# Kernel optimization log

Measured on AMD Instinct MI355X. Metric: run time of the kernel, lower is better.

The kernel has to match this reference:

```python
import jax, jax.numpy as jnp
import numpy as np

OUT_F = 4096
IN_F = 4096
NUM_BITS = 4
BLOCK = 64
R = 16
LORA_SCALE = 32.0 / R  # lora_alpha / r


def setup_inputs() -> dict:
    key = jax.random.key(0)
    k1, k2, k3, k4, k5, k6 = jax.random.split(key, 6)
    n_packed = OUT_F * IN_F * NUM_BITS // 8  # bytes; 2 nibbles per byte
    n_blocks = OUT_F * IN_F // BLOCK
    return {
        "x": jax.random.normal(k1, (2, 1024, IN_F), dtype=jnp.float32),
        "qweight": jax.random.randint(k2, (n_packed,), 0, 256, dtype=jnp.int32),
        "scales": jax.random.uniform(k3, (n_blocks,), dtype=jnp.float32),
        "bias": jax.random.normal(k4, (OUT_F,), dtype=jnp.float32),
        "lora_A": jax.random.normal(k5, (R, IN_F), dtype=jnp.float32) * 0.02,
        "lora_B": jax.random.normal(k6, (OUT_F, R), dtype=jnp.float32) * 0.02,
    }


def _dequantize(qweight, scales):
    # uniform 4-bit lookup table: linspace(-1, 1, 16)
    table = jnp.linspace(-1.0, 1.0, 2 ** NUM_BITS).astype(scales.dtype)
    mask = (1 << NUM_BITS) - 1
    # unpack: index i stored at bits [i*NUM_BITS, (i+1)*NUM_BITS) of each byte
    lo = qweight & mask
    hi = (qweight >> NUM_BITS) & mask
    idx = jnp.stack([lo, hi], axis=-1).reshape(-1)  # [OUT_F*IN_F]
    vals = table[idx]                                # gather from lookup table
    # per-block rescale, then reshape to [OUT_F, IN_F]
    w = vals.reshape(-1, BLOCK) * scales[:, None]
    return w.reshape(OUT_F, IN_F)


def reference(x, qweight, scales, bias, lora_A, lora_B):
    W = _dequantize(qweight, scales)                      # [out, in]
    base = jnp.einsum('bsi,oi->bso', x, W) + bias          # F.linear
    lora = jnp.einsum('bsr,or->bso', jnp.einsum('bsi,ri->bsr', x, lora_A), lora_B)
    return base + LORA_SCALE * lora
```

## Files before the change

kernel.cpp:

```cpp
#include <hip/hip_runtime.h>
#include <hip/hip_bf16.h>
#include <stdint.h>

#define IN_F   4096
#define OUT_F  4096
#define M_ROWS 2048
#define LORA_SCALE 2.0f

typedef __bf16 bf16x8 __attribute__((ext_vector_type(8)));
typedef float  f32x4  __attribute__((ext_vector_type(4)));

typedef const __attribute__((address_space(1))) void gvoid_t;
typedef __attribute__((address_space(3))) void lvoid_t;

__global__ void prep_kernel(const int* __restrict__ qw,
                            const float* __restrict__ scales,
                            __hip_bfloat16* __restrict__ W,
                            const float* __restrict__ x,
                            __hip_bfloat16* __restrict__ xb,
                            const float* __restrict__ A,
                            float* __restrict__ tout) {
    int b = blockIdx.x;
    if (b < 8192) {
        int t = b * 256 + threadIdx.x;
        int4 q = ((const int4*)qw)[t];
        float scale = scales[t >> 3];
        float step = scale * (2.0f / 15.0f);
        int bb[4] = {q.x, q.y, q.z, q.w};
        union { __hip_bfloat16 h[8]; uint4 v; } o;
        #pragma unroll
        for (int j = 0; j < 4; ++j) {
            float lo = (float)(bb[j] & 15)        * step - scale;
            float hi = (float)((bb[j] >> 4) & 15) * step - scale;
            o.h[2*j]   = __float2bfloat16(lo);
            o.h[2*j+1] = __float2bfloat16(hi);
        }
        ((uint4*)W)[t] = o.v;
    } else if (b < 12288) {
        int t = (b - 8192) * 256 + threadIdx.x;
        float4 a = ((const float4*)x)[2*t];
        float4 c = ((const float4*)x)[2*t + 1];
        union { __hip_bfloat16 h[8]; uint4 v; } o;
        o.h[0] = __float2bfloat16(a.x); o.h[1] = __float2bfloat16(a.y);
        o.h[2] = __float2bfloat16(a.z); o.h[3] = __float2bfloat16(a.w);
        o.h[4] = __float2bfloat16(c.x); o.h[5] = __float2bfloat16(c.y);
        o.h[6] = __float2bfloat16(c.z); o.h[7] = __float2bfloat16(c.w);
        ((uint4*)xb)[t] = o.v;
    } else {
        __shared__ float red[16 * 4 * 16];
        int m0 = (b - 12288) * 4;
        int r = threadIdx.x & 15;
        int g = threadIdx.x >> 4;
        float acc[4] = {0.f, 0.f, 0.f, 0.f};
        for (int kb = 0; kb < 64; ++kb) {
            int k = kb * 64 + g * 4;
            float4 av = *(const float4*)(A + (size_t)r * IN_F + k);
            #pragma unroll
            for (int row = 0; row < 4; ++row) {
                float4 xv = *(const float4*)(x + (size_t)(m0 + row) * IN_F + k);
                acc[row] += xv.x*av.x + xv.y*av.y + xv.z*av.z + xv.w*av.w;
            }
        }
        #pragma unroll
        for (int row = 0; row < 4; ++row) red[g*64 + row*16 + r] = acc[row];
        __syncthreads();
        if (threadIdx.x < 64) {
            int row = threadIdx.x >> 4, rr = threadIdx.x & 15;
            float s = 0.f;
            #pragma unroll
            for (int gg = 0; gg < 16; ++gg) s += red[gg*64 + row*16 + rr];
            tout[(size_t)(m0 + row) * 16 + rr] = s;
        }
    }
}

__global__ __launch_bounds__(256) void gemm_kernel(
        const __hip_bfloat16* __restrict__ A,
        const __hip_bfloat16* __restrict__ B,
        const float* __restrict__ bias,
        const float* __restrict__ loraB,
        const float* __restrict__ tmat,
        float* __restrict__ out) {
    const int K = IN_F, N = OUT_F;
    __shared__ union alignas(16) {
        struct { __hip_bfloat16 As[2][128*64]; __hip_bfloat16 Bs[2][128*64]; } s;
        float tstage[128 * 16];
    } sm;

    int tid  = threadIdx.x;
    int wave = tid >> 6, lane = tid & 63;
    int wm = wave >> 1, wn = wave & 1;
    int row16 = lane & 15, quad = lane >> 4;
    int r7 = row16 & 7;
    int m0 = blockIdx.y * 128, n0 = blockIdx.x * 128;

    int rl = lane >> 3;
    int cg = (lane & 7) ^ rl;

    const __hip_bfloat16* pA = A + (size_t)(m0 + wave*32 + rl) * K + cg*8;
    const __hip_bfloat16* pB = B + (size_t)(n0 + wave*32 + rl) * K + cg*8;

    f32x4 acc[4][4];
    #pragma unroll
    for (int i = 0; i < 4; ++i)
        #pragma unroll
        for (int j = 0; j < 4; ++j) acc[i][j] = (f32x4){0.f, 0.f, 0.f, 0.f};

    #pragma unroll
    for (int j = 0; j < 4; ++j) {
        __builtin_amdgcn_global_load_lds((gvoid_t*)(pA + (size_t)j*8*K),
            (lvoid_t*)&sm.s.As[0][(wave*4 + j) * 512], 16, 0, 0);
        __builtin_amdgcn_global_load_lds((gvoid_t*)(pB + (size_t)j*8*K),
            (lvoid_t*)&sm.s.Bs[0][(wave*4 + j) * 512], 16, 0, 0);
    }
    __syncthreads();

    for (int k0 = 0; k0 < K; k0 += 64) {
        int cur = (k0 >> 6) & 1;
        if (k0 + 64 < K) {
            #pragma unroll
            for (int j = 0; j < 4; ++j) {
                __builtin_amdgcn_global_load_lds((gvoid_t*)(pA + k0 + 64 + (size_t)j*8*K),
                    (lvoid_t*)&sm.s.As[cur^1][(wave*4 + j) * 512], 16, 0, 0);
                __builtin_amdgcn_global_load_lds((gvoid_t*)(pB + k0 + 64 + (size_t)j*8*K),
                    (lvoid_t*)&sm.s.Bs[cur^1][(wave*4 + j) * 512], 16, 0, 0);
            }
        }

        #pragma unroll
        for (int s = 0; s < 2; ++s) {
            bf16x8 af[4], bfr[4];
            #pragma unroll
            for (int mt = 0; mt < 4; ++mt) {
                int row = wm*64 + mt*16 + row16;
                af[mt] = *(const bf16x8*)&sm.s.As[cur][row*64 + ((s*4 + quad) ^ r7) * 8];
            }
            #pragma unroll
            for (int nt = 0; nt < 4; ++nt) {
                int row = wn*64 + nt*16 + row16;
                bfr[nt] = *(const bf16x8*)&sm.s.Bs[cur][row*64 + ((s*4 + quad) ^ r7) * 8];
            }
            #pragma unroll
            for (int mt = 0; mt < 4; ++mt)
                #pragma unroll
                for (int nt = 0; nt < 4; ++nt)
                    acc[mt][nt] = __builtin_amdgcn_mfma_f32_16x16x32_bf16(
                        af[mt], bfr[nt], acc[mt][nt], 0, 0, 0);
        }

        __syncthreads();
    }

    #pragma unroll
    for (int i = 0; i < 2; ++i)
        ((float4*)sm.tstage)[tid + i*256] =
            ((const float4*)(tmat + (size_t)m0 * 16))[tid + i*256];
    __syncthreads();

    #pragma unroll
    for (int nt = 0; nt < 4; ++nt) {
        int nl = wn*64 + nt*16 + row16;
        int n  = n0 + nl;
        float bn = bias[n];
        const float4* lb = (const float4*)(loraB + (size_t)n * 16);
        float4 lb0 = lb[0], lb1 = lb[1], lb2 = lb[2], lb3 = lb[3];
        #pragma unroll
        for (int mt = 0; mt < 4; ++mt) {
            #pragma unroll
            for (int r = 0; r < 4; ++r) {
                int ml = wm*64 + mt*16 + quad*4 + r;
                const float* tm = &sm.tstage[ml * 16];
                float dot =
                    tm[0]*lb0.x + tm[1]*lb0.y + tm[2]*lb0.z + tm[3]*lb0.w +
                    tm[4]*lb1.x + tm[5]*lb1.y + tm[6]*lb1.z + tm[7]*lb1.w +
                    tm[8]*lb2.x + tm[9]*lb2.y + tm[10]*lb2.z + tm[11]*lb2.w +
                    tm[12]*lb3.x + tm[13]*lb3.y + tm[14]*lb3.z + tm[15]*lb3.w;
                out[(size_t)(m0 + ml) * N + n] = acc[mt][nt][r] + bn + LORA_SCALE * dot;
            }
        }
    }
}

extern "C" void kernel_launch(void* const* d_in, const int* in_sizes, int n_in,
                              void* d_out, int out_size, void* d_ws, size_t ws_size,
                              hipStream_t stream) {
    const float* x      = (const float*)d_in[0];
    const int*   qw     = (const int*)d_in[1];
    const float* scales = (const float*)d_in[2];
    const float* bias   = (const float*)d_in[3];
    const float* loraA  = (const float*)d_in[4];
    const float* loraB  = (const float*)d_in[5];
    float* out = (float*)d_out;

    char* ws = (char*)d_ws;
    __hip_bfloat16* Wb = (__hip_bfloat16*)ws;
    __hip_bfloat16* Xb = (__hip_bfloat16*)(ws + 33554432);
    float* tmat        = (float*)(ws + 33554432 + 16777216);

    prep_kernel<<<12800, 256, 0, stream>>>(qw, scales, Wb, x, Xb, loraA, tmat);
    gemm_kernel<<<dim3(32, 16), 256, 0, stream>>>(Xb, Wb, bias, loraB, tmat, out);
}
```

Measured before the change: 313.3 us.

## Split GEMM K dimension in two and add separate epilogue reduction kernel

The GEMM grid gains a z dimension that splits K into two halves, which doubles the workgroup count from 512 to 1024 so the CUs are better occupied. The K-tile also shrinks from 64 to 32 with a matching swizzle. Each half writes raw partial sums to its own buffer, and a new epilogue kernel adds the partials, the bias and the LoRA term. In exchange it writes and re-reads an extra 32 MB fp32 partial buffer, adds a kernel launch, and runs twice as many k-loop iterations with half the MFMA work per barrier.

```diff
diff --git a/kernel.cpp b/kernel.cpp
--- a/kernel.cpp
+++ b/kernel.cpp
@@ -77,28 +77,25 @@
 __global__ __launch_bounds__(256) void gemm_kernel(
         const __hip_bfloat16* __restrict__ A,
         const __hip_bfloat16* __restrict__ B,
-        const float* __restrict__ bias,
-        const float* __restrict__ loraB,
-        const float* __restrict__ tmat,
-        float* __restrict__ out) {
+        float* __restrict__ out0,
+        float* __restrict__ p1) {
     const int K = IN_F, N = OUT_F;
-    __shared__ union alignas(16) {
-        struct { __hip_bfloat16 As[2][128*64]; __hip_bfloat16 Bs[2][128*64]; } s;
-        float tstage[128 * 16];
-    } sm;
+    const int KHALF = 2048;
+    __shared__ __hip_bfloat16 As[2][128*32];
+    __shared__ __hip_bfloat16 Bs[2][128*32];
 
     int tid  = threadIdx.x;
     int wave = tid >> 6, lane = tid & 63;
     int wm = wave >> 1, wn = wave & 1;
     int row16 = lane & 15, quad = lane >> 4;
-    int r7 = row16 & 7;
     int m0 = blockIdx.y * 128, n0 = blockIdx.x * 128;
-
-    int rl = lane >> 3;
-    int cg = (lane & 7) ^ rl;
-
-    const __hip_bfloat16* pA = A + (size_t)(m0 + wave*32 + rl) * K + cg*8;
-    const __hip_bfloat16* pB = B + (size_t)(n0 + wave*32 + rl) * K + cg*8;
+    int kb = blockIdx.z * KHALF;
+
+    int rl = lane >> 2;
+    int cg = (lane & 3) ^ ((rl >> 1) & 3);
+
+    const __hip_bfloat16* pA = A + (size_t)(m0 + wave*32 + rl) * K + kb + cg*8;
+    const __hip_bfloat16* pB = B + (size_t)(n0 + wave*32 + rl) * K + kb + cg*8;
 
     f32x4 acc[4][4];
     #pragma unroll
@@ -107,77 +104,90 @@
         for (int j = 0; j < 4; ++j) acc[i][j] = (f32x4){0.f, 0.f, 0.f, 0.f};
 
     #pragma unroll
-    for (int j = 0; j < 4; ++j) {
-        __builtin_amdgcn_global_load_lds((gvoid_t*)(pA + (size_t)j*8*K),
-            (lvoid_t*)&sm.s.As[0][(wave*4 + j) * 512], 16, 0, 0);
-        __builtin_amdgcn_global_load_lds((gvoid_t*)(pB + (size_t)j*8*K),
-            (lvoid_t*)&sm.s.Bs[0][(wave*4 + j) * 512], 16, 0, 0);
+    for (int j = 0; j < 2; ++j) {
+        __builtin_amdgcn_global_load_lds((gvoid_t*)(pA + (size_t)j*16*K),
+            (lvoid_t*)&As[0][(wave*2 + j) * 512], 16, 0, 0);
+        __builtin_amdgcn_global_load_lds((gvoid_t*)(pB + (size_t)j*16*K),
+            (lvoid_t*)&Bs[0][(wave*2 + j) * 512], 16, 0, 0);
     }
     __syncthreads();
 
-    for (int k0 = 0; k0 < K; k0 += 64) {
-        int cur = (k0 >> 6) & 1;
-        if (k0 + 64 < K) {
-            #pragma unroll
-            for (int j = 0; j < 4; ++j) {
-                __builtin_amdgcn_global_load_lds((gvoid_t*)(pA + k0 + 64 + (size_t)j*8*K),
-                    (lvoid_t*)&sm.s.As[cur^1][(wave*4 + j) * 512], 16, 0, 0);
-                __builtin_amdgcn_global_load_lds((gvoid_t*)(pB + k0 + 64 + (size_t)j*8*K),
-                    (lvoid_t*)&sm.s.Bs[cur^1][(wave*4 + j) * 512], 16, 0, 0);
+    for (int k0 = 0; k0 < KHALF; k0 += 32) {
+        int cur = (k0 >> 5) & 1;
+        if (k0 + 32 < KHALF) {
+            #pragma unroll
+            for (int j = 0; j < 2; ++j) {
+                __builtin_amdgcn_global_load_lds((gvoid_t*)(pA + k0 + 32 + (size_t)j*16*K),
+                    (lvoid_t*)&As[cur^1][(wave*2 + j) * 512], 16, 0, 0);
+                __builtin_amdgcn_global_load_lds((gvoid_t*)(pB + k0 + 32 + (size_t)j*16*K),
+                    (lvoid_t*)&Bs[cur^1][(wave*2 + j) * 512], 16, 0, 0);
             }
         }
 
-        #pragma unroll
-        for (int s = 0; s < 2; ++s) {
-            bf16x8 af[4], bfr[4];
-            #pragma unroll
-            for (int mt = 0; mt < 4; ++mt) {
-                int row = wm*64 + mt*16 + row16;
-                af[mt] = *(const bf16x8*)&sm.s.As[cur][row*64 + ((s*4 + quad) ^ r7) * 8];
-            }
-            #pragma unroll
-            for (int nt = 0; nt < 4; ++nt) {
-                int row = wn*64 + nt*16 + row16;
-                bfr[nt] = *(const bf16x8*)&sm.s.Bs[cur][row*64 + ((s*4 + quad) ^ r7) * 8];
-            }
-            #pragma unroll
-            for (int mt = 0; mt < 4; ++mt)
-                #pragma unroll
-                for (int nt = 0; nt < 4; ++nt)
-                    acc[mt][nt] = __builtin_amdgcn_mfma_f32_16x16x32_bf16(
-                        af[mt], bfr[nt], acc[mt][nt], 0, 0, 0);
-        }
+        bf16x8 af[4], bfr[4];
+        #pragma unroll
+        for (int mt = 0; mt < 4; ++mt) {
+            int row = wm*64 + mt*16 + row16;
+            af[mt] = *(const bf16x8*)&As[cur][row*32 + ((quad ^ ((row >> 1) & 3)) << 3)];
+        }
+        #pragma unroll
+        for (int nt = 0; nt < 4; ++nt) {
+            int row = wn*64 + nt*16 + row16;
+            bfr[nt] = *(const bf16x8*)&Bs[cur][row*32 + ((quad ^ ((row >> 1) & 3)) << 3)];
+        }
+        #pragma unroll
+        for (int mt = 0; mt < 4; ++mt)
+            #pragma unroll
+            for (int nt = 0; nt < 4; ++nt)
+                acc[mt][nt] = __builtin_amdgcn_mfma_f32_16x16x32_bf16(
+                    af[mt], bfr[nt], acc[mt][nt], 0, 0, 0);
 
         __syncthreads();
     }
 
-    #pragma unroll
-    for (int i = 0; i < 2; ++i)
-        ((float4*)sm.tstage)[tid + i*256] =
-            ((const float4*)(tmat + (size_t)m0 * 16))[tid + i*256];
-    __syncthreads();
-
+    float* dst = blockIdx.z ? p1 : out0;
     #pragma unroll
     for (int nt = 0; nt < 4; ++nt) {
-        int nl = wn*64 + nt*16 + row16;
-        int n  = n0 + nl;
-        float bn = bias[n];
-        const float4* lb = (const float4*)(loraB + (size_t)n * 16);
-        float4 lb0 = lb[0], lb1 = lb[1], lb2 = lb[2], lb3 = lb[3];
+        int n = n0 + wn*64 + nt*16 + row16;
         #pragma unroll
         for (int mt = 0; mt < 4; ++mt) {
             #pragma unroll
             for (int r = 0; r < 4; ++r) {
                 int ml = wm*64 + mt*16 + quad*4 + r;
-                const float* tm = &sm.tstage[ml * 16];
-                float dot =
-                    tm[0]*lb0.x + tm[1]*lb0.y + tm[2]*lb0.z + tm[3]*lb0.w +
-                    tm[4]*lb1.x + tm[5]*lb1.y + tm[6]*lb1.z + tm[7]*lb1.w +
-                    tm[8]*lb2.x + tm[9]*lb2.y + tm[10]*lb2.z + tm[11]*lb2.w +
-                    tm[12]*lb3.x + tm[13]*lb3.y + tm[14]*lb3.z + tm[15]*lb3.w;
-                out[(size_t)(m0 + ml) * N + n] = acc[mt][nt][r] + bn + LORA_SCALE * dot;
+                dst[(size_t)(m0 + ml) * N + n] = acc[mt][nt][r];
             }
         }
+    }
+}
+
+__global__ __launch_bounds__(256) void epilogue_kernel(
+        float* __restrict__ out, const float* __restrict__ p1,
+        const float* __restrict__ bias, const float* __restrict__ loraB,
+        const float* __restrict__ tmat) {
+    const int N = OUT_F;
+    __shared__ float tl[16 * 16];
+    int m0 = blockIdx.y * 16, n0 = blockIdx.x * 64;
+    int tid = threadIdx.x;
+    if (tid < 64) ((float4*)tl)[tid] = ((const float4*)(tmat + (size_t)m0 * 16))[tid];
+    __syncthreads();
+
+    int nl = tid & 63, mq = tid >> 6;
+    int n = n0 + nl;
+    const float4* lb = (const float4*)(loraB + (size_t)n * 16);
+    float4 b0 = lb[0], b1 = lb[1], b2 = lb[2], b3 = lb[3];
+    float bn = bias[n];
+
+    #pragma unroll
+    for (int j = 0; j < 4; ++j) {
+        int ml = mq * 4 + j;
+        const float* tm = &tl[ml * 16];
+        float dot =
+            tm[0]*b0.x + tm[1]*b0.y + tm[2]*b0.z + tm[3]*b0.w +
+            tm[4]*b1.x + tm[5]*b1.y + tm[6]*b1.z + tm[7]*b1.w +
+            tm[8]*b2.x + tm[9]*b2.y + tm[10]*b2.z + tm[11]*b2.w +
+            tm[12]*b3.x + tm[13]*b3.y + tm[14]*b3.z + tm[15]*b3.w;
+        size_t off = (size_t)(m0 + ml) * N + n;
+        out[off] = out[off] + p1[off] + bn + LORA_SCALE * dot;
     }
 }
 
@@ -195,8 +205,10 @@
     char* ws = (char*)d_ws;
     __hip_bfloat16* Wb = (__hip_bfloat16*)ws;
     __hip_bfloat16* Xb = (__hip_bfloat16*)(ws + 33554432);
-    float* tmat        = (float*)(ws + 33554432 + 16777216);
-
-    prep_kernel<<<12800, 256, 0, stream>>>(qw, scales, Wb, x, Xb, loraA, tmat);
-    gemm_kernel<<<dim3(32, 16), 256, 0, stream>>>(Xb, Wb, bias, loraB, tmat, out);
-}
+    float* tmat        = (float*)(ws + 50331648);
+    float* p1          = (float*)(ws + 50462720);
+
+    prep_kernel    <<<12800, 256, 0, stream>>>(qw, scales, Wb, x, Xb, loraA, tmat);
+    gemm_kernel    <<<dim3(32, 16, 2), 256, 0, stream>>>(Xb, Wb, out, p1);
+    epilogue_kernel<<<dim3(64, 128), 256, 0, stream>>>(out, p1, bias, loraB, tmat);
+}
```

Result: faster. 296.8 us (-5.3%).
